# Optimization experiments

Measured on AMD Instinct MI355X. Metric: run time of the kernel, lower is better.

The kernel has to match this reference:

```python
import jax, jax.numpy as jnp
import numpy as np

N = 50000
E = 600000
IN = 128
HID = 128
OUT = 64
EPS = 1e-5


def layernorm(x, g, b):
    mu = jnp.mean(x, axis=-1, keepdims=True)
    var = jnp.mean(jnp.square(x - mu), axis=-1, keepdims=True)
    return (x - mu) * jax.lax.rsqrt(var + EPS) * g + b


def film_layer(x, W, Fm, g, b, src, dst):
    # x: [N, d_in]; W: [d_out, d_in]; Fm: [2*d_out, d_in]
    m = x @ W.T                       # [N, d_out]
    fw = x @ Fm.T                     # [N, 2*d_out]
    d_out = W.shape[0]
    gamma, beta = fw[:, :d_out], fw[:, d_out:]
    msg = jax.nn.relu(gamma * m + beta)           # [N, d_out]
    h = jax.ops.segment_sum(msg[src], dst, num_segments=N)  # scatter-sum over edges
    return layernorm(h, g, b)  # dropout is identity in eval mode


def setup_inputs() -> dict:
    key = jax.random.key(0)
    ks = jax.random.split(key, 12)
    s = lambda fan_in: 1.0 / np.sqrt(fan_in)
    return {
        "features": jax.random.normal(ks[0], (N, IN), dtype=jnp.float32),
        "src": jax.random.randint(ks[1], (E,), 0, N, dtype=jnp.int32),
        "dst": jax.random.randint(ks[2], (E,), 0, N, dtype=jnp.int32),
        "W1": jax.random.uniform(ks[3], (HID, IN), jnp.float32, -s(IN), s(IN)),
        "F1": jax.random.uniform(ks[4], (2 * HID, IN), jnp.float32, -s(IN), s(IN)),
        "g1": jnp.ones((HID,), jnp.float32),
        "b1": jnp.zeros((HID,), jnp.float32),
        "W2": jax.random.uniform(ks[5], (HID, HID), jnp.float32, -s(HID), s(HID)),
        "F2": jax.random.uniform(ks[6], (2 * HID, HID), jnp.float32, -s(HID), s(HID)),
        "g2": jnp.ones((HID,), jnp.float32),
        "b2": jnp.zeros((HID,), jnp.float32),
        "Wp": jax.random.uniform(ks[7], (OUT, HID), jnp.float32, -s(HID), s(HID)),
        "bp": jax.random.uniform(ks[8], (OUT,), jnp.float32, -s(HID), s(HID)),
    }


def reference(features, src, dst, W1, F1, g1, b1, W2, F2, g2, b2, Wp, bp):
    h = film_layer(features, W1, F1, g1, b1, src, dst)
    h = film_layer(h, W2, F2, g2, b2, src, dst)
    return jax.nn.sigmoid(h @ Wp.T + bp)  # [N, OUT]
```

## Files before the change

kernel.cpp:

```cpp
#include <hip/hip_runtime.h>
#include <hip/hip_bf16.h>
#include <math.h>

#define IN_D 128
#define HID_D 128
#define OUT_D 64
#define CAP 64

typedef __attribute__((ext_vector_type(8))) short bf16x8;
typedef __attribute__((ext_vector_type(4))) float f32x4;

__device__ __forceinline__ unsigned short f2bf(float f) {
    unsigned u = __float_as_uint(f);
    u += 0x7fffu + ((u >> 16) & 1u);
    return (unsigned short)(u >> 16);
}
__device__ __forceinline__ float bf2f(unsigned short h) {
    return __uint_as_float(((unsigned)h) << 16);
}

__global__ __launch_bounds__(256) void k_prep_fill(
        const int* __restrict__ src_idx, const int* __restrict__ dst_idx,
        int* __restrict__ cnt, unsigned short* __restrict__ elist,
        int E, int W, int range,
        const float* __restrict__ W1, const float* __restrict__ F1,
        const float* __restrict__ W2, const float* __restrict__ F2,
        const float* __restrict__ Wp,
        const float* __restrict__ X, unsigned short* __restrict__ fx, int nfv,
        unsigned short* __restrict__ wc1, unsigned short* __restrict__ wc2,
        unsigned short* __restrict__ wpb) {
    int e = blockIdx.x * 256 + threadIdx.x;
    if (e < nfv) {
        const float4* xp = (const float4*)X + (size_t)e * 4;
        float4 v0 = xp[0], v1 = xp[1], v2 = xp[2], v3 = xp[3];
        uint4 o0, o1;
        o0.x = (unsigned)f2bf(v0.x) | ((unsigned)f2bf(v0.y) << 16);
        o0.y = (unsigned)f2bf(v0.z) | ((unsigned)f2bf(v0.w) << 16);
        o0.z = (unsigned)f2bf(v1.x) | ((unsigned)f2bf(v1.y) << 16);
        o0.w = (unsigned)f2bf(v1.z) | ((unsigned)f2bf(v1.w) << 16);
        o1.x = (unsigned)f2bf(v2.x) | ((unsigned)f2bf(v2.y) << 16);
        o1.y = (unsigned)f2bf(v2.z) | ((unsigned)f2bf(v2.w) << 16);
        o1.z = (unsigned)f2bf(v3.x) | ((unsigned)f2bf(v3.y) << 16);
        o1.w = (unsigned)f2bf(v3.z) | ((unsigned)f2bf(v3.w) << 16);
        ((uint4*)fx)[(size_t)e * 2]     = o0;
        ((uint4*)fx)[(size_t)e * 2 + 1] = o1;
    }
    const int NW = HID_D * IN_D;
    const int NC = 3 * NW;
    const int NP = OUT_D * HID_D;
    int i = e;
    if (i < NC) {
        wc1[i] = f2bf(i < NW ? W1[i] : F1[i - NW]);
    } else if (i < 2 * NC) {
        int j = i - NC;
        wc2[j] = f2bf(j < NW ? W2[j] : F2[j - NW]);
    } else if (i < 2 * NC + NP) {
        int j = i - 2 * NC;
        wpb[j] = f2bf(Wp[j]);
    }

    const int g = blockIdx.x & 7;
    const int sub = blockIdx.x >> 3;
    const int lo = g * range;
    const int base = sub * W;
    int end = base + W;
    if (end > E) end = E;
    for (int ed = base + threadIdx.x; ed < end; ed += 256) {
        int d = dst_idx[ed];
        int s = src_idx[ed];
        if ((unsigned)(d - lo) < (unsigned)range) {
            int pos = atomicAdd(&cnt[d], 1);
            elist[(size_t)d * CAP + pos] = (unsigned short)s;
        }
    }
}

__global__ __launch_bounds__(256, 2) void k_msg(const unsigned short* __restrict__ X,
                                                const unsigned short* __restrict__ Wc,
                                                unsigned short* __restrict__ Msg,
                                                int n, int nchunks) {
    const int wave = threadIdx.x >> 6;
    const int lane = threadIdx.x & 63;
    const int lr = lane & 15;
    const int quad = lane >> 4;
    const int t0 = wave * 2;
    const int tidx[6] = {t0, t0 + 1, t0 + 8, t0 + 9, t0 + 16, t0 + 17};

    bf16x8 b[6][4];
    #pragma unroll
    for (int u = 0; u < 6; u++)
        #pragma unroll
        for (int s = 0; s < 4; s++)
            b[u][s] = *(const bf16x8*)(Wc + (size_t)(16 * tidx[u] + lr) * IN_D + quad * 8 + 32 * s);

    for (int c = blockIdx.x; c < nchunks; c += gridDim.x) {
        const int row0 = c << 4;

        int r = row0 + lr;
        if (r > n - 1) r = n - 1;
        const unsigned short* xp = X + (size_t)r * IN_D + quad * 8;
        bf16x8 a[4];
        #pragma unroll
        for (int s = 0; s < 4; s++) a[s] = *(const bf16x8*)(xp + 32 * s);

        f32x4 acc[6];
        #pragma unroll
        for (int u = 0; u < 6; u++) acc[u] = (f32x4){0.f, 0.f, 0.f, 0.f};

        #pragma unroll
        for (int s = 0; s < 4; s++)
            #pragma unroll
            for (int u = 0; u < 6; u++)
                acc[u] = __builtin_amdgcn_mfma_f32_16x16x32_bf16(a[s], b[u][s], acc[u], 0, 0, 0);

        #pragma unroll
        for (int u = 0; u < 2; u++) {
            #pragma unroll
            for (int rr = 0; rr < 4; rr++) {
                int row = row0 + quad * 4 + rr;
                if (row < n) {
                    float v = acc[2 + u][rr] * acc[u][rr] + acc[4 + u][rr];
                    v = v > 0.f ? v : 0.f;
                    Msg[(size_t)row * HID_D + 16 * (t0 + u) + lr] = f2bf(v);
                }
            }
        }
    }
}

__global__ __launch_bounds__(256) void k_agg_ln(const unsigned short* __restrict__ Msg,
                                                const unsigned short* __restrict__ elist,
                                                const int* __restrict__ cnt,
                                                const float* __restrict__ gamma,
                                                const float* __restrict__ beta,
                                                unsigned short* __restrict__ Hout, int n) {
    int node = blockIdx.x * 4 + (threadIdx.x >> 6);
    int lane = threadIdx.x & 63;
    int g = lane >> 4;
    int l16 = lane & 15;
    if (node >= n) return;
    const unsigned short* seg = elist + (size_t)node * CAP;
    int deg = cnt[node];
    int myidx = seg[lane];
    float a0 = 0.f, a1 = 0.f, a2 = 0.f, a3 = 0.f;
    float a4 = 0.f, a5 = 0.f, a6 = 0.f, a7 = 0.f;

#define ACC8(v) { a0 += bf2f((unsigned short)((v).x & 0xffffu)); \
                  a1 += bf2f((unsigned short)((v).x >> 16));     \
                  a2 += bf2f((unsigned short)((v).y & 0xffffu)); \
                  a3 += bf2f((unsigned short)((v).y >> 16));     \
                  a4 += bf2f((unsigned short)((v).z & 0xffffu)); \
                  a5 += bf2f((unsigned short)((v).z >> 16));     \
                  a6 += bf2f((unsigned short)((v).w & 0xffffu)); \
                  a7 += bf2f((unsigned short)((v).w >> 16)); }

    int i = 0;
    for (; i + 8 <= deg; i += 8) {
        int iA = __shfl(myidx, i + g);
        int iB = __shfl(myidx, i + 4 + g);
        uint4 vA = *(const uint4*)(Msg + (size_t)iA * HID_D + l16 * 8);
        uint4 vB = *(const uint4*)(Msg + (size_t)iB * HID_D + l16 * 8);
        ACC8(vA);
        ACC8(vB);
    }
    if (i + 4 <= deg) {
        int iA = __shfl(myidx, i + g);
        uint4 vA = *(const uint4*)(Msg + (size_t)iA * HID_D + l16 * 8);
        ACC8(vA);
        i += 4;
    }
    int rem = deg - i;
    if (rem) {
        int iA = __shfl(myidx, i + (g < rem ? g : 0));
        if (g < rem) {
            uint4 vA = *(const uint4*)(Msg + (size_t)iA * HID_D + l16 * 8);
            ACC8(vA);
        }
    }
#undef ACC8

    a0 += __shfl_xor(a0, 16); a1 += __shfl_xor(a1, 16);
    a2 += __shfl_xor(a2, 16); a3 += __shfl_xor(a3, 16);
    a4 += __shfl_xor(a4, 16); a5 += __shfl_xor(a5, 16);
    a6 += __shfl_xor(a6, 16); a7 += __shfl_xor(a7, 16);
    a0 += __shfl_xor(a0, 32); a1 += __shfl_xor(a1, 32);
    a2 += __shfl_xor(a2, 32); a3 += __shfl_xor(a3, 32);
    a4 += __shfl_xor(a4, 32); a5 += __shfl_xor(a5, 32);
    a6 += __shfl_xor(a6, 32); a7 += __shfl_xor(a7, 32);

    float s  = a0 + a1 + a2 + a3 + a4 + a5 + a6 + a7;
    float sq = a0 * a0 + a1 * a1 + a2 * a2 + a3 * a3
             + a4 * a4 + a5 * a5 + a6 * a6 + a7 * a7;
    #pragma unroll
    for (int d = 8; d; d >>= 1) {
        s += __shfl_xor(s, d);
        sq += __shfl_xor(sq, d);
    }
    float mu = s * (1.f / 128.f);
    float var = sq * (1.f / 128.f) - mu * mu;
    float rs = rsqrtf(var + 1e-5f);

    if (g == 0) {
        float4 g0 = ((const float4*)gamma)[l16 * 2];
        float4 g1 = ((const float4*)gamma)[l16 * 2 + 1];
        float4 b0 = ((const float4*)beta)[l16 * 2];
        float4 b1 = ((const float4*)beta)[l16 * 2 + 1];
        float y0 = (a0 - mu) * rs * g0.x + b0.x;
        float y1 = (a1 - mu) * rs * g0.y + b0.y;
        float y2 = (a2 - mu) * rs * g0.z + b0.z;
        float y3 = (a3 - mu) * rs * g0.w + b0.w;
        float y4 = (a4 - mu) * rs * g1.x + b1.x;
        float y5 = (a5 - mu) * rs * g1.y + b1.y;
        float y6 = (a6 - mu) * rs * g1.z + b1.z;
        float y7 = (a7 - mu) * rs * g1.w + b1.w;
        uint4 o;
        o.x = (unsigned)f2bf(y0) | ((unsigned)f2bf(y1) << 16);
        o.y = (unsigned)f2bf(y2) | ((unsigned)f2bf(y3) << 16);
        o.z = (unsigned)f2bf(y4) | ((unsigned)f2bf(y5) << 16);
        o.w = (unsigned)f2bf(y6) | ((unsigned)f2bf(y7) << 16);
        *(uint4*)(Hout + (size_t)node * HID_D + l16 * 8) = o;
    }
}

__global__ __launch_bounds__(256) void k_proj(const unsigned short* __restrict__ H,
                                              const unsigned short* __restrict__ Wpb,
                                              const float* __restrict__ bp,
                                              float* __restrict__ out, int n) {
    const int row0 = blockIdx.x << 6;
    const int wave = threadIdx.x >> 6;
    const int lane = threadIdx.x & 63;
    const int lr = lane & 15;
    const int quad = lane >> 4;

    f32x4 acc[4];
    #pragma unroll
    for (int rt = 0; rt < 4; rt++) acc[rt] = (f32x4){0.f, 0.f, 0.f, 0.f};

    #pragma unroll
    for (int s = 0; s < 4; s++) {
        bf16x8 bv = *(const bf16x8*)(Wpb + (size_t)(16 * wave + lr) * HID_D + quad * 8 + 32 * s);
        #pragma unroll
        for (int rt = 0; rt < 4; rt++) {
            int r = row0 + rt * 16 + lr;
            if (r > n - 1) r = n - 1;
            bf16x8 av = *(const bf16x8*)(H + (size_t)r * HID_D + quad * 8 + 32 * s);
            acc[rt] = __builtin_amdgcn_mfma_f32_16x16x32_bf16(av, bv, acc[rt], 0, 0, 0);
        }
    }
    float bias = bp[16 * wave + lr];
    #pragma unroll
    for (int rt = 0; rt < 4; rt++) {
        #pragma unroll
        for (int r = 0; r < 4; r++) {
            int row = row0 + rt * 16 + quad * 4 + r;
            if (row < n) {
                float z = acc[rt][r] + bias;
                out[(size_t)row * OUT_D + 16 * wave + lr] = 1.f / (1.f + __expf(-z));
            }
        }
    }
}

extern "C" void kernel_launch(void* const* d_in, const int* in_sizes, int n_in,
                              void* d_out, int out_size, void* d_ws, size_t ws_size,
                              hipStream_t stream) {
    const float* features = (const float*)d_in[0];
    const int* src = (const int*)d_in[1];
    const int* dst = (const int*)d_in[2];
    const float* W1 = (const float*)d_in[3];
    const float* F1 = (const float*)d_in[4];
    const float* g1 = (const float*)d_in[5];
    const float* b1 = (const float*)d_in[6];
    const float* W2 = (const float*)d_in[7];
    const float* F2 = (const float*)d_in[8];
    const float* g2 = (const float*)d_in[9];
    const float* b2 = (const float*)d_in[10];
    const float* Wp = (const float*)d_in[11];
    const float* bp = (const float*)d_in[12];

    const int N = in_sizes[0] / IN_D;
    const int E = in_sizes[1];
    float* out = (float*)d_out;

    char* p = (char*)d_ws;
    auto alloc = [&](size_t b) -> char* {
        char* r = p;
        p += (b + 255) & ~(size_t)255;
        return r;
    };
    unsigned short* buf0 = (unsigned short*)alloc((size_t)N * HID_D * 2);
    unsigned short* buf1 = (unsigned short*)alloc((size_t)N * HID_D * 2);
    unsigned short* fx   = (unsigned short*)alloc((size_t)N * IN_D * 2);
    unsigned short* wc1  = (unsigned short*)alloc((size_t)3 * HID_D * IN_D * 2);
    unsigned short* wc2  = (unsigned short*)alloc((size_t)3 * HID_D * HID_D * 2);
    unsigned short* wpb  = (unsigned short*)alloc((size_t)OUT_D * HID_D * 2);
    int* cnt    = (int*)alloc((size_t)N * 4);
    unsigned short* elist = (unsigned short*)alloc((size_t)N * CAP * 2);

    const int mc = (N + 15) / 16;
    const int mg = 512;
    const int pb = (N + 63) / 64;
    const int ab = (N + 3) / 4;
    const int nfv = (N * IN_D) / 16;
    const int fb = 2048;
    const int W = (E + 255) / 256;
    const int range = (N + 7) / 8;

    hipMemsetAsync(cnt, 0, (size_t)N * 4, stream);
    k_prep_fill<<<fb, 256, 0, stream>>>(src, dst, cnt, elist, E, W, range,
                                        W1, F1, W2, F2, Wp,
                                        features, fx, nfv, wc1, wc2, wpb);

    k_msg<<<mg, 256, 0, stream>>>(fx, wc1, buf1, N, mc);
    k_agg_ln<<<ab, 256, 0, stream>>>(buf1, elist, cnt, g1, b1, buf0, N);
    k_msg<<<mg, 256, 0, stream>>>(buf0, wc2, buf1, N, mc);
    k_agg_ln<<<ab, 256, 0, stream>>>(buf1, elist, cnt, g2, b2, buf0, N);
    k_proj<<<pb, 256, 0, stream>>>(buf0, wpb, bp, out, N);
}
```

Before: 225.3 us.

## Fuse output projection and sigmoid into second aggregation-layernorm kernel

The final projection (128->64 matmul plus bias and sigmoid) moves into the second k_agg_ln via a template flag. Each wave broadcasts its normalized row through shuffles and computes one output column per lane with scalar FMAs, which removes the bf16 H write and re-read and one launch. In exchange, the MFMA matmul becomes 128 shuffles and FMAs per node, plus a per-lane weight-row load. k_msg also changes its grid from a fixed 512 to half the tile count.

New measurement: 313.0 us. 1.39x slower.

```diff
diff --git a/kernel.cpp b/kernel.cpp
--- a/kernel.cpp
+++ b/kernel.cpp
@@ -128,12 +128,17 @@
     }
 }
 
+template <int PROJ>
 __global__ __launch_bounds__(256) void k_agg_ln(const unsigned short* __restrict__ Msg,
                                                 const unsigned short* __restrict__ elist,
                                                 const int* __restrict__ cnt,
                                                 const float* __restrict__ gamma,
                                                 const float* __restrict__ beta,
-                                                unsigned short* __restrict__ Hout, int n) {
+                                                unsigned short* __restrict__ Hout,
+                                                int n,
+                                                const unsigned short* __restrict__ Wpb,
+                                                const float* __restrict__ bp,
+                                                float* __restrict__ out) {
     int node = blockIdx.x * 4 + (threadIdx.x >> 6);
     int lane = threadIdx.x & 63;
     int g = lane >> 4;
@@ -200,63 +205,50 @@
     float var = sq * (1.f / 128.f) - mu * mu;
     float rs = rsqrtf(var + 1e-5f);
 
-    if (g == 0) {
-        float4 g0 = ((const float4*)gamma)[l16 * 2];
-        float4 g1 = ((const float4*)gamma)[l16 * 2 + 1];
-        float4 b0 = ((const float4*)beta)[l16 * 2];
-        float4 b1 = ((const float4*)beta)[l16 * 2 + 1];
-        float y0 = (a0 - mu) * rs * g0.x + b0.x;
-        float y1 = (a1 - mu) * rs * g0.y + b0.y;
-        float y2 = (a2 - mu) * rs * g0.z + b0.z;
-        float y3 = (a3 - mu) * rs * g0.w + b0.w;
-        float y4 = (a4 - mu) * rs * g1.x + b1.x;
-        float y5 = (a5 - mu) * rs * g1.y + b1.y;
-        float y6 = (a6 - mu) * rs * g1.z + b1.z;
-        float y7 = (a7 - mu) * rs * g1.w + b1.w;
-        uint4 o;
-        o.x = (unsigned)f2bf(y0) | ((unsigned)f2bf(y1) << 16);
-        o.y = (unsigned)f2bf(y2) | ((unsigned)f2bf(y3) << 16);
-        o.z = (unsigned)f2bf(y4) | ((unsigned)f2bf(y5) << 16);
-        o.w = (unsigned)f2bf(y6) | ((unsigned)f2bf(y7) << 16);
-        *(uint4*)(Hout + (size_t)node * HID_D + l16 * 8) = o;
-    }
-}
-
-__global__ __launch_bounds__(256) void k_proj(const unsigned short* __restrict__ H,
-                                              const unsigned short* __restrict__ Wpb,
-                                              const float* __restrict__ bp,
-                                              float* __restrict__ out, int n) {
-    const int row0 = blockIdx.x << 6;
-    const int wave = threadIdx.x >> 6;
-    const int lane = threadIdx.x & 63;
-    const int lr = lane & 15;
-    const int quad = lane >> 4;
-
-    f32x4 acc[4];
-    #pragma unroll
-    for (int rt = 0; rt < 4; rt++) acc[rt] = (f32x4){0.f, 0.f, 0.f, 0.f};
-
-    #pragma unroll
-    for (int s = 0; s < 4; s++) {
-        bf16x8 bv = *(const bf16x8*)(Wpb + (size_t)(16 * wave + lr) * HID_D + quad * 8 + 32 * s);
-        #pragma unroll
-        for (int rt = 0; rt < 4; rt++) {
-            int r = row0 + rt * 16 + lr;
-            if (r > n - 1) r = n - 1;
-            bf16x8 av = *(const bf16x8*)(H + (size_t)r * HID_D + quad * 8 + 32 * s);
-            acc[rt] = __builtin_amdgcn_mfma_f32_16x16x32_bf16(av, bv, acc[rt], 0, 0, 0);
-        }
-    }
-    float bias = bp[16 * wave + lr];
-    #pragma unroll
-    for (int rt = 0; rt < 4; rt++) {
-        #pragma unroll
-        for (int r = 0; r < 4; r++) {
-            int row = row0 + rt * 16 + quad * 4 + r;
-            if (row < n) {
-                float z = acc[rt][r] + bias;
-                out[(size_t)row * OUT_D + 16 * wave + lr] = 1.f / (1.f + __expf(-z));
-            }
+    float4 gg0 = ((const float4*)gamma)[l16 * 2];
+    float4 gg1 = ((const float4*)gamma)[l16 * 2 + 1];
+    float4 bb0 = ((const float4*)beta)[l16 * 2];
+    float4 bb1 = ((const float4*)beta)[l16 * 2 + 1];
+    float y0 = (a0 - mu) * rs * gg0.x + bb0.x;
+    float y1 = (a1 - mu) * rs * gg0.y + bb0.y;
+    float y2 = (a2 - mu) * rs * gg0.z + bb0.z;
+    float y3 = (a3 - mu) * rs * gg0.w + bb0.w;
+    float y4 = (a4 - mu) * rs * gg1.x + bb1.x;
+    float y5 = (a5 - mu) * rs * gg1.y + bb1.y;
+    float y6 = (a6 - mu) * rs * gg1.z + bb1.z;
+    float y7 = (a7 - mu) * rs * gg1.w + bb1.w;
+
+    if (PROJ) {
+        float acc = bp[lane];
+        #pragma unroll
+        for (int j = 0; j < 16; j++) {
+            float h0 = __shfl(y0, j);
+            float h1 = __shfl(y1, j);
+            float h2 = __shfl(y2, j);
+            float h3 = __shfl(y3, j);
+            float h4 = __shfl(y4, j);
+            float h5 = __shfl(y5, j);
+            float h6 = __shfl(y6, j);
+            float h7 = __shfl(y7, j);
+            bf16x8 w = *(const bf16x8*)(Wpb + (size_t)lane * HID_D + j * 8);
+            acc += h0 * bf2f((unsigned short)w[0]);
+            acc += h1 * bf2f((unsigned short)w[1]);
+            acc += h2 * bf2f((unsigned short)w[2]);
+            acc += h3 * bf2f((unsigned short)w[3]);
+            acc += h4 * bf2f((unsigned short)w[4]);
+            acc += h5 * bf2f((unsigned short)w[5]);
+            acc += h6 * bf2f((unsigned short)w[6]);
+            acc += h7 * bf2f((unsigned short)w[7]);
+        }
+        out[(size_t)node * OUT_D + lane] = 1.f / (1.f + __expf(-acc));
+    } else {
+        if (g == 0) {
+            uint4 o;
+            o.x = (unsigned)f2bf(y0) | ((unsigned)f2bf(y1) << 16);
+            o.y = (unsigned)f2bf(y2) | ((unsigned)f2bf(y3) << 16);
+            o.z = (unsigned)f2bf(y4) | ((unsigned)f2bf(y5) << 16);
+            o.w = (unsigned)f2bf(y6) | ((unsigned)f2bf(y7) << 16);
+            *(uint4*)(Hout + (size_t)node * HID_D + l16 * 8) = o;
         }
     }
 }
@@ -298,8 +290,7 @@
     unsigned short* elist = (unsigned short*)alloc((size_t)N * CAP * 2);
 
     const int mc = (N + 15) / 16;
-    const int mg = 512;
-    const int pb = (N + 63) / 64;
+    const int mg = (mc + 1) / 2;
     const int ab = (N + 3) / 4;
     const int nfv = (N * IN_D) / 16;
     const int fb = 2048;
@@ -312,8 +303,9 @@
                                         features, fx, nfv, wc1, wc2, wpb);
 
     k_msg<<<mg, 256, 0, stream>>>(fx, wc1, buf1, N, mc);
-    k_agg_ln<<<ab, 256, 0, stream>>>(buf1, elist, cnt, g1, b1, buf0, N);
+    k_agg_ln<0><<<ab, 256, 0, stream>>>(buf1, elist, cnt, g1, b1, buf0, N,
+                                        nullptr, nullptr, nullptr);
     k_msg<<<mg, 256, 0, stream>>>(buf0, wc2, buf1, N, mc);
-    k_agg_ln<<<ab, 256, 0, stream>>>(buf1, elist, cnt, g2, b2, buf0, N);
-    k_proj<<<pb, 256, 0, stream>>>(buf0, wpb, bp, out, N);
-}
+    k_agg_ln<1><<<ab, 256, 0, stream>>>(buf1, elist, cnt, g2, b2, nullptr, N,
+                                        wpb, bp, out);
+}
```

## Widen aggregation gather batches and raise k_msg occupancy and grid size

Applied to the files above, without the earlier changes.

The aggregation loop now issues four independent 16-byte gathers per lane per iteration, covering 16 edges per wave step, with predicated tails in place of the separate 8/4/remainder paths. This is meant to raise memory-level parallelism in the gather. k_msg's launch bounds go from 2 to 4 blocks per SM, and its grid is sized to about half the chunk count instead of a fixed 512. The higher occupancy target may force register spills, since k_msg holds 24 preloaded bf16x8 weight fragments per thread, and the larger grid repeats those weight loads in more blocks.

Result: slower. 271.7 us (+20.6%).

```diff
diff --git a/kernel.cpp b/kernel.cpp
--- a/kernel.cpp
+++ b/kernel.cpp
@@ -75,7 +75,7 @@
     }
 }
 
-__global__ __launch_bounds__(256, 2) void k_msg(const unsigned short* __restrict__ X,
+__global__ __launch_bounds__(256, 4) void k_msg(const unsigned short* __restrict__ X,
                                                 const unsigned short* __restrict__ Wc,
                                                 unsigned short* __restrict__ Msg,
                                                 int n, int nchunks) {
@@ -136,7 +136,7 @@
                                                 unsigned short* __restrict__ Hout, int n) {
     int node = blockIdx.x * 4 + (threadIdx.x >> 6);
     int lane = threadIdx.x & 63;
-    int g = lane >> 4;
+    int g4 = lane >> 4;
     int l16 = lane & 15;
     if (node >= n) return;
     const unsigned short* seg = elist + (size_t)node * CAP;
@@ -154,28 +154,22 @@
                   a6 += bf2f((unsigned short)((v).w & 0xffffu)); \
                   a7 += bf2f((unsigned short)((v).w >> 16)); }
 
-    int i = 0;
-    for (; i + 8 <= deg; i += 8) {
-        int iA = __shfl(myidx, i + g);
-        int iB = __shfl(myidx, i + 4 + g);
-        uint4 vA = *(const uint4*)(Msg + (size_t)iA * HID_D + l16 * 8);
-        uint4 vB = *(const uint4*)(Msg + (size_t)iB * HID_D + l16 * 8);
-        ACC8(vA);
-        ACC8(vB);
-    }
-    if (i + 4 <= deg) {
-        int iA = __shfl(myidx, i + g);
-        uint4 vA = *(const uint4*)(Msg + (size_t)iA * HID_D + l16 * 8);
-        ACC8(vA);
-        i += 4;
-    }
-    int rem = deg - i;
-    if (rem) {
-        int iA = __shfl(myidx, i + (g < rem ? g : 0));
-        if (g < rem) {
-            uint4 vA = *(const uint4*)(Msg + (size_t)iA * HID_D + l16 * 8);
-            ACC8(vA);
-        }
+    const int r0 = g4, r1 = g4 + 4, r2 = g4 + 8, r3 = g4 + 12;
+    for (int i = 0; i < deg; i += 16) {
+        int nbat = deg - i; if (nbat > 16) nbat = 16;
+        int s0 = __shfl(myidx, i + (r0 < nbat ? r0 : 0));
+        int s1 = __shfl(myidx, i + (r1 < nbat ? r1 : 0));
+        int s2 = __shfl(myidx, i + (r2 < nbat ? r2 : 0));
+        int s3 = __shfl(myidx, i + (r3 < nbat ? r3 : 0));
+        uint4 v0, v1, v2, v3;
+        if (r0 < nbat) v0 = *(const uint4*)(Msg + (size_t)s0 * HID_D + l16 * 8);
+        if (r1 < nbat) v1 = *(const uint4*)(Msg + (size_t)s1 * HID_D + l16 * 8);
+        if (r2 < nbat) v2 = *(const uint4*)(Msg + (size_t)s2 * HID_D + l16 * 8);
+        if (r3 < nbat) v3 = *(const uint4*)(Msg + (size_t)s3 * HID_D + l16 * 8);
+        if (r0 < nbat) ACC8(v0);
+        if (r1 < nbat) ACC8(v1);
+        if (r2 < nbat) ACC8(v2);
+        if (r3 < nbat) ACC8(v3);
     }
 #undef ACC8
 
@@ -200,7 +194,7 @@
     float var = sq * (1.f / 128.f) - mu * mu;
     float rs = rsqrtf(var + 1e-5f);
 
-    if (g == 0) {
+    if (g4 == 0) {
         float4 g0 = ((const float4*)gamma)[l16 * 2];
         float4 g1 = ((const float4*)gamma)[l16 * 2 + 1];
         float4 b0 = ((const float4*)beta)[l16 * 2];
@@ -298,7 +292,7 @@
     unsigned short* elist = (unsigned short*)alloc((size_t)N * CAP * 2);
 
     const int mc = (N + 15) / 16;
-    const int mg = 512;
+    const int mg = (mc + 1) / 2;
     const int pb = (N + 63) / 64;
     const int ab = (N + 3) / 4;
     const int nfv = (N * IN_D) / 16;
```
